# Kernel tuning notes

Measured on AMD Instinct MI355X. Metric: run time of the kernel, lower is better.

Reference implementation:

```python
import jax, jax.numpy as jnp
import numpy as np

LN_EPS = 1e-5


def layer_norm(x, gamma, beta):
    mu = jnp.mean(x, axis=-1, keepdims=True)
    var = jnp.mean(jnp.square(x - mu), axis=-1, keepdims=True)
    return (x - mu) * jax.lax.rsqrt(var + LN_EPS) * gamma + beta


def setup_inputs() -> dict:
    key = jax.random.key(0)
    ks = jax.random.split(key, 4)
    b, t, d, h, r = 4, 2048, 1024, 4096, 32
    x = jax.random.normal(ks[0], (b, t, d), dtype=jnp.float32)
    L = jax.random.normal(ks[1], (d, r), dtype=jnp.float32) * (1.0 / np.sqrt(d))
    W1 = jax.random.normal(ks[2], (d, h), dtype=jnp.float32) * (1.0 / np.sqrt(d))
    W2 = jax.random.normal(ks[3], (h, d), dtype=jnp.float32) * (1.0 / np.sqrt(h))
    return {
        "x": x, "L": L,
        "W1": W1, "b1": jnp.zeros((h,), jnp.float32),
        "W2": W2, "b2": jnp.zeros((d,), jnp.float32),
        "gamma1": jnp.ones((d,), jnp.float32), "beta1": jnp.zeros((d,), jnp.float32),
        "gamma2": jnp.ones((d,), jnp.float32), "beta2": jnp.zeros((d,), jnp.float32),
    }


def reference(x, L, W1, b1, W2, b2, gamma1, beta1, gamma2, beta2):
    d = x.shape[-1]
    # --- GeodesicAttention on norm1(x) ---
    hn = layer_norm(x, gamma1, beta1)  # (b,t,d)
    g = jnp.eye(d, dtype=x.dtype) + L @ L.T  # PSD metric G = I + L L^T, (d,d)
    # dist_sq[b,i,j] = (x_i - x_j)^T G (x_i - x_j)
    #               = q_i + q_j - 2 x_i^T G x_j   (quadratic expansion; avoids (b,t,t,d) diff tensor)
    xg = jnp.einsum('btd,de->bte', hn, g)          # G x, (b,t,d)
    q = jnp.einsum('btd,btd->bt', xg, hn)          # diag quadratic form, (b,t)
    cross = jnp.einsum('bid,bjd->bij', xg, hn)     # x_i^T G x_j, (b,t,t)
    dist_sq = q[:, :, None] + q[:, None, :] - 2.0 * cross
    attn = jax.nn.softmax(-dist_sq, axis=-1)       # (b,t,t)
    x = x + jnp.einsum('bij,bjd->bid', attn, hn)
    # --- MLP on norm2(x) ---
    hm = layer_norm(x, gamma2, beta2)
    hid = jax.nn.gelu(hm @ W1 + b1, approximate=False)
    x = x + hid @ W2 + b2
    return x
```

## Files before the change

kernel.cpp:

```cpp
#include <hip/hip_runtime.h>
#include <cstdint>

typedef float f32x4 __attribute__((ext_vector_type(4)));
typedef __bf16 bf16x8 __attribute__((ext_vector_type(8)));

#define AS1 __attribute__((address_space(1)))
#define AS3 __attribute__((address_space(3)))

__device__ __forceinline__ void gld_lds16(const void* g, void* l) {
    __builtin_amdgcn_global_load_lds((const AS1 void*)g, (AS3 void*)l, 16, 0, 0);
}

__device__ __forceinline__ unsigned short f2bf(float f) {
    unsigned u = __builtin_bit_cast(unsigned, f);
    u = u + 0x7fffu + ((u >> 16) & 1u);
    return (unsigned short)(u >> 16);
}
__device__ __forceinline__ float bf2f(unsigned short h) {
    unsigned u = ((unsigned)h) << 16;
    return __builtin_bit_cast(float, u);
}

template<int MODE>
__global__ __launch_bounds__(256) void gemm_nt(
    const unsigned short* __restrict__ A, long lda, long sAb,
    const unsigned short* __restrict__ B, long ldb, long sBb,
    void* C, long ldc, long sCb,
    const float* add, long ldadd, long sAddb,
    const float* __restrict__ bias,
    int K)
{
    __shared__ char smA[128 * 64 * 2];
    __shared__ char smB[128 * 64 * 2];
    const int tid  = threadIdx.x;
    const int lane = tid & 63, wid = tid >> 6;
    const int wr = wid >> 1, wc = wid & 1;
    const long zb = blockIdx.z;

    const int nwg  = gridDim.x * gridDim.y;
    const int orig = blockIdx.y * gridDim.x + blockIdx.x;
    const int q8 = nwg >> 3, r8 = nwg & 7;
    const int xcd = orig & 7;
    const int wg  = (xcd < r8 ? xcd * (q8 + 1) : r8 * (q8 + 1) + (xcd - r8) * q8) + (orig >> 3);
    const int bx = wg % gridDim.x, by = wg / gridDim.x;

    const char* Ab = (const char*)(A + zb * sAb + (long)by * 128 * lda);
    const char* Bb = (const char*)(B + zb * sBb + (long)bx * 128 * ldb);
    const long lda2 = lda * 2, ldb2 = ldb * 2;
    const int srow = lane >> 3;
    const int scol = (lane & 7) * 16;

    f32x4 acc[4][4] = {};
    for (int k0 = 0; k0 < K; k0 += 64) {
        if (k0) __syncthreads();
        const long kb = (long)k0 * 2;
#pragma unroll
        for (int i = 0; i < 4; ++i) {
            const int seg = i * 4 + wid;
            const int r = seg * 8 + srow;
            gld_lds16(Ab + (long)r * lda2 + kb + scol, smA + seg * 1024);
            gld_lds16(Bb + (long)r * ldb2 + kb + scol, smB + seg * 1024);
        }
        __syncthreads();
#pragma unroll
        for (int kk = 0; kk < 2; ++kk) {
            bf16x8 af[4], bfm[4];
#pragma unroll
            for (int m = 0; m < 4; ++m)
                af[m] = *(const bf16x8*)(smA + (wr * 64 + m * 16 + (lane & 15)) * 128 + kk * 64 + (lane >> 4) * 16);
#pragma unroll
            for (int n = 0; n < 4; ++n)
                bfm[n] = *(const bf16x8*)(smB + (wc * 64 + n * 16 + (lane & 15)) * 128 + kk * 64 + (lane >> 4) * 16);
#pragma unroll
            for (int m = 0; m < 4; ++m)
#pragma unroll
                for (int n = 0; n < 4; ++n)
                    acc[m][n] = __builtin_amdgcn_mfma_f32_16x16x32_bf16(af[m], bfm[n], acc[m][n], 0, 0, 0);
        }
    }
    const long row0 = (long)by * 128 + wr * 64 + (lane >> 4) * 4;
    const long col0 = (long)bx * 128 + wc * 64 + (lane & 15);
#pragma unroll
    for (int m = 0; m < 4; ++m)
#pragma unroll
        for (int n = 0; n < 4; ++n)
#pragma unroll
            for (int j = 0; j < 4; ++j) {
                const long r = row0 + m * 16 + j;
                const long c = col0 + n * 16;
                const float v = acc[m][n][j];
                if (MODE == 0) {
                    ((float*)C)[zb * sCb + r * ldc + c] = v;
                } else if (MODE == 1) {
                    ((float*)C)[zb * sCb + r * ldc + c] = v + add[zb * sAddb + r * ldadd + c];
                } else if (MODE == 2) {
                    float t = v + bias[c];
                    float gl = 0.5f * t * (1.0f + erff(t * 0.70710678118654752f));
                    ((unsigned short*)C)[zb * sCb + r * ldc + c] = f2bf(gl);
                } else {
                    ((float*)C)[zb * sCb + r * ldc + c] = v + bias[c] + add[zb * sAddb + r * ldadd + c];
                }
            }
}

__global__ __launch_bounds__(256) void ln_kernel(
    const float* __restrict__ x, const float* __restrict__ gamma, const float* __restrict__ beta,
    unsigned short* __restrict__ out, int ldout, float* qout, int pad)
{
    const int tid = threadIdx.x;
    const long row = blockIdx.x;
    float4 v = ((const float4*)(x + row * 1024))[tid];
    float s = v.x + v.y + v.z + v.w;
    float s2 = v.x * v.x + v.y * v.y + v.z * v.z + v.w * v.w;
#pragma unroll
    for (int off = 32; off; off >>= 1) {
        s  += __shfl_down(s, off);
        s2 += __shfl_down(s2, off);
    }
    __shared__ float red[12];
    const int lane = tid & 63, wid = tid >> 6;
    if (lane == 0) { red[wid] = s; red[4 + wid] = s2; }
    __syncthreads();
    s  = red[0] + red[1] + red[2] + red[3];
    s2 = red[4] + red[5] + red[6] + red[7];
    const float mu = s * (1.0f / 1024.0f);
    const float var = s2 * (1.0f / 1024.0f) - mu * mu;
    const float rs = rsqrtf(var + 1e-5f);
    const float4 g = ((const float4*)gamma)[tid];
    const float4 b = ((const float4*)beta)[tid];
    unsigned short o0 = f2bf((v.x - mu) * rs * g.x + b.x);
    unsigned short o1 = f2bf((v.y - mu) * rs * g.y + b.y);
    unsigned short o2 = f2bf((v.z - mu) * rs * g.z + b.z);
    unsigned short o3 = f2bf((v.w - mu) * rs * g.w + b.w);
    ushort4 ov; ov.x = o0; ov.y = o1; ov.z = o2; ov.w = o3;
    ((ushort4*)(out + row * (long)ldout))[tid] = ov;
    if (pad && tid < 32) out[row * (long)ldout + 1056 + tid] = 0;
    if (qout) {
        float y0 = bf2f(o0), y1 = bf2f(o1), y2 = bf2f(o2), y3 = bf2f(o3);
        float sq = y0 * y0 + y1 * y1 + y2 * y2 + y3 * y3;
#pragma unroll
        for (int off = 32; off; off >>= 1) sq += __shfl_down(sq, off);
        if (lane == 0) red[8 + wid] = sq;
        __syncthreads();
        if (tid == 0) qout[row] = red[8] + red[9] + red[10] + red[11];
    }
}

__global__ __launch_bounds__(256) void u_kernel(
    unsigned short* __restrict__ z, const float* __restrict__ L, float* __restrict__ q)
{
    const int tid = threadIdx.x;
    const long row = blockIdx.x;
    __shared__ float hn[1024];
    __shared__ float part[8][32];
    ushort4 uv = ((const ushort4*)(z + row * 1088))[tid];
    hn[tid * 4 + 0] = bf2f(uv.x);
    hn[tid * 4 + 1] = bf2f(uv.y);
    hn[tid * 4 + 2] = bf2f(uv.z);
    hn[tid * 4 + 3] = bf2f(uv.w);
    __syncthreads();
    const int j = tid & 31, grp = tid >> 5;
    float acc = 0.f;
    const float* Lp = L + j;
#pragma unroll 4
    for (int d = grp * 128; d < grp * 128 + 128; ++d)
        acc += hn[d] * Lp[(long)d * 32];
    part[grp][j] = acc;
    __syncthreads();
    if (tid < 32) {
        float u = 0.f;
#pragma unroll
        for (int g2 = 0; g2 < 8; ++g2) u += part[g2][tid];
        unsigned short ub = f2bf(u);
        z[row * 1088 + 1024 + tid] = ub;
        float uf = bf2f(ub);
        part[0][tid] = uf * uf;
    }
    __syncthreads();
    if (tid == 0) {
        float sq = 0.f;
#pragma unroll
        for (int t2 = 0; t2 < 32; ++t2) sq += part[0][t2];
        q[row] += sq;
    }
}

__global__ __launch_bounds__(256) void softmax_kernel(
    float* S, const float* qb)
{
    const int tid = threadIdx.x;
    const long i = blockIdx.x, bl = blockIdx.y;
    float* Sr = S + (bl * 2048 + i) * 2048;
    const float* qr = qb + bl * 2048;
    float l[8];
    float mx = -1e30f;
#pragma unroll
    for (int c2 = 0; c2 < 8; ++c2) {
        const int jj = tid + c2 * 256;
        l[c2] = 2.0f * Sr[jj] - qr[jj];
        mx = fmaxf(mx, l[c2]);
    }
#pragma unroll
    for (int off = 32; off; off >>= 1) mx = fmaxf(mx, __shfl_xor(mx, off));
    __shared__ float red[8];
    const int lane = tid & 63, wid = tid >> 6;
    if (lane == 0) red[wid] = mx;
    __syncthreads();
    mx = fmaxf(fmaxf(red[0], red[1]), fmaxf(red[2], red[3]));
    float sum = 0.f;
#pragma unroll
    for (int c2 = 0; c2 < 8; ++c2) { l[c2] = __expf(l[c2] - mx); sum += l[c2]; }
#pragma unroll
    for (int off = 32; off; off >>= 1) sum += __shfl_xor(sum, off);
    if (lane == 0) red[4 + wid] = sum;
    __syncthreads();
    sum = red[4] + red[5] + red[6] + red[7];
    const float inv = 1.0f / sum;
    unsigned short* Pr = (unsigned short*)S + (bl * 2048 + i) * 4096;
#pragma unroll
    for (int c2 = 0; c2 < 8; ++c2)
        Pr[tid + c2 * 256] = f2bf(l[c2] * inv);
}

__global__ __launch_bounds__(256) void transpose_v_kernel(
    const unsigned short* __restrict__ z, unsigned short* __restrict__ Vt, long sVtb)
{
    __shared__ unsigned short t[32][33];
    const int tid = threadIdx.x;
    const int tx = tid & 31, ty = tid >> 5;
    const long b = blockIdx.z;
    const long k0 = (long)blockIdx.x * 32, n0 = (long)blockIdx.y * 32;
#pragma unroll
    for (int r = 0; r < 32; r += 8)
        t[r + ty][tx] = z[(b * 2048 + k0 + r + ty) * 1088 + n0 + tx];
    __syncthreads();
#pragma unroll
    for (int r = 0; r < 32; r += 8)
        Vt[b * sVtb + (n0 + r + ty) * 2048 + k0 + tx] = t[tx][r + ty];
}

__global__ __launch_bounds__(256) void cast_transpose_kernel(
    const float* __restrict__ W, unsigned short* __restrict__ Wt, int rows, int cols)
{
    __shared__ float t[32][33];
    const int tid = threadIdx.x;
    const int tx = tid & 31, ty = tid >> 5;
    const long r0 = (long)blockIdx.y * 32, c0 = (long)blockIdx.x * 32;
#pragma unroll
    for (int r = 0; r < 32; r += 8)
        t[r + ty][tx] = W[(r0 + r + ty) * (long)cols + c0 + tx];
    __syncthreads();
#pragma unroll
    for (int r = 0; r < 32; r += 8)
        Wt[(c0 + r + ty) * (long)rows + r0 + tx] = f2bf(t[tx][r + ty]);
}

extern "C" void kernel_launch(void* const* d_in, const int* in_sizes, int n_in,
                              void* d_out, int out_size, void* d_ws, size_t ws_size,
                              hipStream_t stream)
{
    const float* x   = (const float*)d_in[0];
    const float* L   = (const float*)d_in[1];
    const float* W1  = (const float*)d_in[2];
    const float* b1  = (const float*)d_in[3];
    const float* W2  = (const float*)d_in[4];
    const float* b2  = (const float*)d_in[5];
    const float* g1  = (const float*)d_in[6];
    const float* be1 = (const float*)d_in[7];
    const float* g2  = (const float*)d_in[8];
    const float* be2 = (const float*)d_in[9];
    float* out = (float*)d_out;
    unsigned short* z = (unsigned short*)d_out;

    char* wsp = (char*)d_ws;
    float* q = (float*)wsp;
    char* pool = wsp + 32768;
    unsigned short* Vt   = (unsigned short*)pool;
    float*          Smat = (float*)(pool + 16777216);
    unsigned short* W1t = (unsigned short*)pool;
    unsigned short* W2t = (unsigned short*)(pool + 8388608);
    unsigned short* hm  = (unsigned short*)(pool + 16777216);
    unsigned short* hid = (unsigned short*)(pool + 33554432);
    const bool fullMLP = ws_size >= (size_t)32768 + 100663296 + 65536;

    ln_kernel<<<8192, 256, 0, stream>>>(x, g1, be1, z, 1088, q, 1);
    u_kernel<<<8192, 256, 0, stream>>>(z, L, q);

    transpose_v_kernel<<<dim3(64, 32, 4), 256, 0, stream>>>(z, Vt, (long)1024 * 2048);
    gemm_nt<0><<<dim3(16, 16, 4), 256, 0, stream>>>(
        z, 1088, (long)2048 * 1088,
        z, 1088, (long)2048 * 1088,
        Smat, 2048, (long)2048 * 2048,
        nullptr, 0, 0, nullptr, 1088);
    softmax_kernel<<<dim3(2048, 4), 256, 0, stream>>>(Smat, q);
    gemm_nt<1><<<dim3(8, 16, 4), 256, 0, stream>>>(
        (const unsigned short*)Smat, 4096, (long)2048 * 4096,
        Vt, 2048, (long)1024 * 2048,
        out, 1024, (long)2048 * 1024,
        x, 1024, (long)2048 * 1024,
        nullptr, 2048);

    cast_transpose_kernel<<<dim3(128, 32), 256, 0, stream>>>(W1, W1t, 1024, 4096);
    cast_transpose_kernel<<<dim3(32, 128), 256, 0, stream>>>(W2, W2t, 4096, 1024);
    ln_kernel<<<8192, 256, 0, stream>>>(out, g2, be2, hm, 1024, nullptr, 0);
    if (fullMLP) {
        gemm_nt<2><<<dim3(32, 64, 1), 256, 0, stream>>>(
            hm, 1024, 0, W1t, 1024, 0,
            hid, 4096, 0, nullptr, 0, 0, b1, 1024);
        gemm_nt<3><<<dim3(8, 64, 1), 256, 0, stream>>>(
            hid, 4096, 0, W2t, 4096, 0,
            out, 1024, 0, out, 1024, 0, b2, 4096);
    } else {
        for (int c = 0; c < 2; ++c) {
            const unsigned short* hmc = hm + (size_t)c * 4096 * 1024;
            float* oc = out + (size_t)c * 4096 * 1024;
            gemm_nt<2><<<dim3(32, 32, 1), 256, 0, stream>>>(
                hmc, 1024, 0, W1t, 1024, 0,
                hid, 4096, 0, nullptr, 0, 0, b1, 1024);
            gemm_nt<3><<<dim3(8, 32, 1), 256, 0, stream>>>(
                hid, 4096, 0, W2t, 4096, 0,
                oc, 1024, 0, oc, 1024, 0, b2, 4096);
        }
    }
}
```

Measured before the change: 425.1 us.

## Replace GEMM with 256-row tiles, 512 threads and 4-stage async LDS pipeline

Replaces the single-buffered 128x128 GEMM with a 256xBN tile kernel that runs 8 waves per block and keeps four K=32 stages in LDS. Loads are issued ahead and waited on through explicit vmcnt counts. MFMA blocks are wrapped in setprio so global loads overlap compute and the per-tile barrier stalls go away. The larger tiles raise data reuse per load. In exchange the kernel uses more LDS and registers, and correctness depends on hand-counted vmcnt values and on K being a multiple of 32.

```diff
diff --git a/kernel.cpp b/kernel.cpp
--- a/kernel.cpp
+++ b/kernel.cpp
@@ -21,22 +21,27 @@
     return __builtin_bit_cast(float, u);
 }
 
-template<int MODE>
-__global__ __launch_bounds__(256) void gemm_nt(
+__device__ __forceinline__ void bar() {
+    asm volatile("" ::: "memory");
+    __builtin_amdgcn_s_barrier();
+    asm volatile("" ::: "memory");
+}
+
+template<int BN, int MODE>
+__global__ __launch_bounds__(512, 2) void gemm_nt2(
     const unsigned short* __restrict__ A, long lda, long sAb,
     const unsigned short* __restrict__ B, long ldb, long sBb,
     void* C, long ldc, long sCb,
     const float* add, long ldadd, long sAddb,
-    const float* __restrict__ bias,
-    int K)
-{
-    __shared__ char smA[128 * 64 * 2];
-    __shared__ char smB[128 * 64 * 2];
-    const int tid  = threadIdx.x;
-    const int lane = tid & 63, wid = tid >> 6;
-    const int wr = wid >> 1, wc = wid & 1;
+    const float* __restrict__ bias, int K)
+{
+    constexpr int NR  = BN / 64;
+    constexpr int BUF = 16384 + BN * 64;
+    __shared__ char sm[4 * BUF];
+    const int tid = threadIdx.x, lane = tid & 63, wid = tid >> 6;
+    const int wr = wid >> 2, wc = wid & 3;
+
     const long zb = blockIdx.z;
-
     const int nwg  = gridDim.x * gridDim.y;
     const int orig = blockIdx.y * gridDim.x + blockIdx.x;
     const int q8 = nwg >> 3, r8 = nwg & 7;
@@ -44,46 +49,74 @@
     const int wg  = (xcd < r8 ? xcd * (q8 + 1) : r8 * (q8 + 1) + (xcd - r8) * q8) + (orig >> 3);
     const int bx = wg % gridDim.x, by = wg / gridDim.x;
 
-    const char* Ab = (const char*)(A + zb * sAb + (long)by * 128 * lda);
-    const char* Bb = (const char*)(B + zb * sBb + (long)bx * 128 * ldb);
-    const long lda2 = lda * 2, ldb2 = ldb * 2;
-    const int srow = lane >> 3;
-    const int scol = (lane & 7) * 16;
-
-    f32x4 acc[4][4] = {};
-    for (int k0 = 0; k0 < K; k0 += 64) {
-        if (k0) __syncthreads();
-        const long kb = (long)k0 * 2;
-#pragma unroll
-        for (int i = 0; i < 4; ++i) {
-            const int seg = i * 4 + wid;
-            const int r = seg * 8 + srow;
-            gld_lds16(Ab + (long)r * lda2 + kb + scol, smA + seg * 1024);
-            gld_lds16(Bb + (long)r * ldb2 + kb + scol, smB + seg * 1024);
+    const char* Ab = (const char*)(A + zb * sAb + (long)by * 256 * lda);
+    const char* Bb = (const char*)(B + zb * sBb + (long)bx * BN * ldb);
+    const long ldaB = lda * 2, ldbB = ldb * 2;
+    const int  grow = tid >> 2;
+    const long gcol = (long)(tid & 3) * 16;
+
+    auto stage = [&](int kt, int bi) {
+        const char* As = Ab + (long)kt * 64 + gcol;
+        const char* Bs = Bb + (long)kt * 64 + gcol;
+        char* d = sm + bi * BUF + wid * 1024;
+#pragma unroll
+        for (int i = 0; i < 2; ++i)
+            gld_lds16(As + (long)(i * 128 + grow) * ldaB, d + i * 8192);
+#pragma unroll
+        for (int i = 0; i < BN / 128; ++i)
+            gld_lds16(Bs + (long)(i * 128 + grow) * ldbB, d + 16384 + i * 8192);
+    };
+
+    f32x4 acc[8][NR] = {};
+    const int NT = K / 32;
+    stage(0, 0);
+    if (NT > 1) stage(1, 1);
+    if (NT > 2) stage(2, 2);
+
+    for (int t = 0; t < NT; ++t) {
+        const int rem = NT - t;
+        if (rem > 3) {
+            stage(t + 3, (t + 3) & 3);
+            if constexpr (BN == 256) asm volatile("s_waitcnt vmcnt(12)" ::: "memory");
+            else                     asm volatile("s_waitcnt vmcnt(9)"  ::: "memory");
+        } else if (rem == 3) {
+            if constexpr (BN == 256) asm volatile("s_waitcnt vmcnt(8)" ::: "memory");
+            else                     asm volatile("s_waitcnt vmcnt(6)" ::: "memory");
+        } else if (rem == 2) {
+            if constexpr (BN == 256) asm volatile("s_waitcnt vmcnt(4)" ::: "memory");
+            else                     asm volatile("s_waitcnt vmcnt(3)" ::: "memory");
+        } else {
+            asm volatile("s_waitcnt vmcnt(0)" ::: "memory");
         }
-        __syncthreads();
-#pragma unroll
-        for (int kk = 0; kk < 2; ++kk) {
-            bf16x8 af[4], bfm[4];
-#pragma unroll
-            for (int m = 0; m < 4; ++m)
-                af[m] = *(const bf16x8*)(smA + (wr * 64 + m * 16 + (lane & 15)) * 128 + kk * 64 + (lane >> 4) * 16);
-#pragma unroll
-            for (int n = 0; n < 4; ++n)
-                bfm[n] = *(const bf16x8*)(smB + (wc * 64 + n * 16 + (lane & 15)) * 128 + kk * 64 + (lane >> 4) * 16);
-#pragma unroll
-            for (int m = 0; m < 4; ++m)
-#pragma unroll
-                for (int n = 0; n < 4; ++n)
-                    acc[m][n] = __builtin_amdgcn_mfma_f32_16x16x32_bf16(af[m], bfm[n], acc[m][n], 0, 0, 0);
-        }
-    }
-    const long row0 = (long)by * 128 + wr * 64 + (lane >> 4) * 4;
-    const long col0 = (long)bx * 128 + wc * 64 + (lane & 15);
-#pragma unroll
-    for (int m = 0; m < 4; ++m)
-#pragma unroll
-        for (int n = 0; n < 4; ++n)
+        bar();
+
+        const char* bufA = sm + (t & 3) * BUF;
+        const char* bufB = bufA + 16384;
+        bf16x8 af[8], bfr[NR];
+#pragma unroll
+        for (int m = 0; m < 8; ++m)
+            af[m] = *(const bf16x8*)(bufA + (wr * 128 + m * 16 + (lane & 15)) * 64 + (lane >> 4) * 16);
+#pragma unroll
+        for (int n = 0; n < NR; ++n)
+            bfr[n] = *(const bf16x8*)(bufB + (wc * 16 * NR + n * 16 + (lane & 15)) * 64 + (lane >> 4) * 16);
+        __builtin_amdgcn_s_setprio(1);
+#pragma unroll
+        for (int m = 0; m < 8; ++m)
+#pragma unroll
+            for (int n = 0; n < NR; ++n)
+                acc[m][n] = __builtin_amdgcn_mfma_f32_16x16x32_bf16(af[m], bfr[n], acc[m][n], 0, 0, 0);
+        __builtin_amdgcn_s_setprio(0);
+        asm volatile("s_waitcnt lgkmcnt(0)" ::: "memory");
+        __builtin_amdgcn_sched_barrier(0);
+        bar();
+    }
+
+    const long row0 = (long)by * 256 + wr * 128 + (lane >> 4) * 4;
+    const long col0 = (long)bx * BN + wc * 16 * NR + (lane & 15);
+#pragma unroll
+    for (int m = 0; m < 8; ++m)
+#pragma unroll
+        for (int n = 0; n < NR; ++n)
 #pragma unroll
             for (int j = 0; j < 4; ++j) {
                 const long r = row0 + m * 16 + j;
@@ -94,8 +127,8 @@
                 } else if (MODE == 1) {
                     ((float*)C)[zb * sCb + r * ldc + c] = v + add[zb * sAddb + r * ldadd + c];
                 } else if (MODE == 2) {
-                    float t = v + bias[c];
-                    float gl = 0.5f * t * (1.0f + erff(t * 0.70710678118654752f));
+                    float tt = v + bias[c];
+                    float gl = 0.5f * tt * (1.0f + erff(tt * 0.70710678118654752f));
                     ((unsigned short*)C)[zb * sCb + r * ldc + c] = f2bf(gl);
                 } else {
                     ((float*)C)[zb * sCb + r * ldc + c] = v + bias[c] + add[zb * sAddb + r * ldadd + c];
@@ -287,13 +320,13 @@
     u_kernel<<<8192, 256, 0, stream>>>(z, L, q);
 
     transpose_v_kernel<<<dim3(64, 32, 4), 256, 0, stream>>>(z, Vt, (long)1024 * 2048);
-    gemm_nt<0><<<dim3(16, 16, 4), 256, 0, stream>>>(
+    gemm_nt2<256, 0><<<dim3(8, 8, 4), 512, 0, stream>>>(
         z, 1088, (long)2048 * 1088,
         z, 1088, (long)2048 * 1088,
         Smat, 2048, (long)2048 * 2048,
         nullptr, 0, 0, nullptr, 1088);
     softmax_kernel<<<dim3(2048, 4), 256, 0, stream>>>(Smat, q);
-    gemm_nt<1><<<dim3(8, 16, 4), 256, 0, stream>>>(
+    gemm_nt2<128, 1><<<dim3(8, 8, 4), 512, 0, stream>>>(
         (const unsigned short*)Smat, 4096, (long)2048 * 4096,
         Vt, 2048, (long)1024 * 2048,
         out, 1024, (long)2048 * 1024,
@@ -304,20 +337,20 @@
     cast_transpose_kernel<<<dim3(32, 128), 256, 0, stream>>>(W2, W2t, 4096, 1024);
     ln_kernel<<<8192, 256, 0, stream>>>(out, g2, be2, hm, 1024, nullptr, 0);
     if (fullMLP) {
-        gemm_nt<2><<<dim3(32, 64, 1), 256, 0, stream>>>(
+        gemm_nt2<256, 2><<<dim3(16, 32, 1), 512, 0, stream>>>(
             hm, 1024, 0, W1t, 1024, 0,
             hid, 4096, 0, nullptr, 0, 0, b1, 1024);
-        gemm_nt<3><<<dim3(8, 64, 1), 256, 0, stream>>>(
+        gemm_nt2<128, 3><<<dim3(8, 32, 1), 512, 0, stream>>>(
             hid, 4096, 0, W2t, 4096, 0,
             out, 1024, 0, out, 1024, 0, b2, 4096);
     } else {
         for (int c = 0; c < 2; ++c) {
             const unsigned short* hmc = hm + (size_t)c * 4096 * 1024;
             float* oc = out + (size_t)c * 4096 * 1024;
-            gemm_nt<2><<<dim3(32, 32, 1), 256, 0, stream>>>(
+            gemm_nt2<256, 2><<<dim3(16, 16, 1), 512, 0, stream>>>(
                 hmc, 1024, 0, W1t, 1024, 0,
                 hid, 4096, 0, nullptr, 0, 0, b1, 1024);
-            gemm_nt<3><<<dim3(8, 32, 1), 256, 0, stream>>>(
+            gemm_nt2<128, 3><<<dim3(8, 16, 1), 512, 0, stream>>>(
                 hid, 4096, 0, W2t, 4096, 0,
                 oc, 1024, 0, oc, 1024, 0, b2, 4096);
         }
```

New measurement: 392.8 us. 1.08x faster.

## Triple-buffer GEMM K-loop with async LDS loads and swizzled shared layout

Applied to the files above, without the earlier changes.

Rewrites the bf16 MFMA GEMM main loop to use a 3-stage LDS ring buffer with a K step of 32. Global-to-LDS loads for tile t+2 are issued before the MFMAs on tile t, and explicit vmcnt waits replace the double syncthreads per iteration. It also adds an XOR swizzle on the LDS layout to cut bank conflicts, raises wave priority around the MFMA block, and sets an occupancy hint of 3 blocks per CU. The aim is to hide global memory latency behind compute. In exchange it uses more shared memory and depends on hand-tuned waitcnt counts being correct.

```diff
diff --git a/kernel.cpp b/kernel.cpp
--- a/kernel.cpp
+++ b/kernel.cpp
@@ -21,22 +21,31 @@
     return __builtin_bit_cast(float, u);
 }
 
+__device__ __forceinline__ void bar() {
+    asm volatile("" ::: "memory");
+    __builtin_amdgcn_s_barrier();
+    asm volatile("" ::: "memory");
+}
+
+#define WAITVM(n) asm volatile("s_waitcnt vmcnt(" #n ")" ::: "memory")
+#define LGKM0     asm volatile("s_waitcnt lgkmcnt(0)" ::: "memory")
+#define SCHED0    __builtin_amdgcn_sched_barrier(0)
+
 template<int MODE>
-__global__ __launch_bounds__(256) void gemm_nt(
+__global__ __launch_bounds__(256, 3) void gemm128(
     const unsigned short* __restrict__ A, long lda, long sAb,
     const unsigned short* __restrict__ B, long ldb, long sBb,
     void* C, long ldc, long sCb,
     const float* add, long ldadd, long sAddb,
-    const float* __restrict__ bias,
-    int K)
-{
-    __shared__ char smA[128 * 64 * 2];
-    __shared__ char smB[128 * 64 * 2];
-    const int tid  = threadIdx.x;
-    const int lane = tid & 63, wid = tid >> 6;
+    const float* __restrict__ bias, int K)
+{
+    constexpr int ABUF = 128 * 64;
+    constexpr int BUF  = 2 * ABUF;
+    __shared__ char sm[3 * BUF];
+    const int tid = threadIdx.x, lane = tid & 63, wid = tid >> 6;
     const int wr = wid >> 1, wc = wid & 1;
+
     const long zb = blockIdx.z;
-
     const int nwg  = gridDim.x * gridDim.y;
     const int orig = blockIdx.y * gridDim.x + blockIdx.x;
     const int q8 = nwg >> 3, r8 = nwg & 7;
@@ -46,38 +55,58 @@
 
     const char* Ab = (const char*)(A + zb * sAb + (long)by * 128 * lda);
     const char* Bb = (const char*)(B + zb * sBb + (long)bx * 128 * ldb);
-    const long lda2 = lda * 2, ldb2 = ldb * 2;
-    const int srow = lane >> 3;
-    const int scol = (lane & 7) * 16;
+    const long ldaB = lda * 2, ldbB = ldb * 2;
+
+    const long gsw = (long)(((tid & 3) ^ ((tid >> 3) & 3)) << 4);
+    auto stage = [&](int kt, int b) {
+#pragma unroll
+        for (int i = 0; i < 2; ++i) {
+            const int r = i * 64 + (tid >> 2);
+            gld_lds16(Ab + (long)r * ldaB + (long)kt * 64 + gsw,
+                      sm + b * BUF + i * 4096 + wid * 1024);
+            gld_lds16(Bb + (long)r * ldbB + (long)kt * 64 + gsw,
+                      sm + b * BUF + ABUF + i * 4096 + wid * 1024);
+        }
+    };
 
     f32x4 acc[4][4] = {};
-    for (int k0 = 0; k0 < K; k0 += 64) {
-        if (k0) __syncthreads();
-        const long kb = (long)k0 * 2;
-#pragma unroll
-        for (int i = 0; i < 4; ++i) {
-            const int seg = i * 4 + wid;
-            const int r = seg * 8 + srow;
-            gld_lds16(Ab + (long)r * lda2 + kb + scol, smA + seg * 1024);
-            gld_lds16(Bb + (long)r * ldb2 + kb + scol, smB + seg * 1024);
-        }
-        __syncthreads();
-#pragma unroll
-        for (int kk = 0; kk < 2; ++kk) {
-            bf16x8 af[4], bfm[4];
-#pragma unroll
-            for (int m = 0; m < 4; ++m)
-                af[m] = *(const bf16x8*)(smA + (wr * 64 + m * 16 + (lane & 15)) * 128 + kk * 64 + (lane >> 4) * 16);
+    const int NT = K / 32;
+    const int cc = ((lane >> 4) ^ ((lane >> 1) & 3)) << 4;
+
+    stage(0, 0); stage(1, 1);
+    WAITVM(4);
+    bar();
+
+#pragma unroll 1
+    for (int t = 0; t < NT; ++t) {
+        const char* bufp = sm + (t % 3) * BUF;
+        bf16x8 af[4], bfr[4];
+#pragma unroll
+        for (int m = 0; m < 4; ++m) {
+            const int R = wr * 64 + m * 16 + (lane & 15);
+            af[m] = *(const bf16x8*)(bufp + R * 64 + cc);
+        }
+#pragma unroll
+        for (int n = 0; n < 4; ++n) {
+            const int R = wc * 64 + n * 16 + (lane & 15);
+            bfr[n] = *(const bf16x8*)(bufp + ABUF + R * 64 + cc);
+        }
+        if (t + 2 < NT) stage(t + 2, (t + 2) % 3);
+        LGKM0; SCHED0;
+        __builtin_amdgcn_s_setprio(1);
+#pragma unroll
+        for (int m = 0; m < 4; ++m)
 #pragma unroll
             for (int n = 0; n < 4; ++n)
-                bfm[n] = *(const bf16x8*)(smB + (wc * 64 + n * 16 + (lane & 15)) * 128 + kk * 64 + (lane >> 4) * 16);
-#pragma unroll
-            for (int m = 0; m < 4; ++m)
-#pragma unroll
-                for (int n = 0; n < 4; ++n)
-                    acc[m][n] = __builtin_amdgcn_mfma_f32_16x16x32_bf16(af[m], bfm[n], acc[m][n], 0, 0, 0);
-        }
-    }
+                acc[m][n] = __builtin_amdgcn_mfma_f32_16x16x32_bf16(
+                    af[m], bfr[n], acc[m][n], 0, 0, 0);
+        __builtin_amdgcn_s_setprio(0);
+        if (t + 1 < NT) {
+            if (t + 2 < NT) WAITVM(4); else WAITVM(0);
+            bar();
+        }
+    }
+
     const long row0 = (long)by * 128 + wr * 64 + (lane >> 4) * 4;
     const long col0 = (long)bx * 128 + wc * 64 + (lane & 15);
 #pragma unroll
@@ -94,8 +123,8 @@
                 } else if (MODE == 1) {
                     ((float*)C)[zb * sCb + r * ldc + c] = v + add[zb * sAddb + r * ldadd + c];
                 } else if (MODE == 2) {
-                    float t = v + bias[c];
-                    float gl = 0.5f * t * (1.0f + erff(t * 0.70710678118654752f));
+                    float tt = v + bias[c];
+                    float gl = 0.5f * tt * (1.0f + erff(tt * 0.70710678118654752f));
                     ((unsigned short*)C)[zb * sCb + r * ldc + c] = f2bf(gl);
                 } else {
                     ((float*)C)[zb * sCb + r * ldc + c] = v + bias[c] + add[zb * sAddb + r * ldadd + c];
@@ -287,13 +316,13 @@
     u_kernel<<<8192, 256, 0, stream>>>(z, L, q);
 
     transpose_v_kernel<<<dim3(64, 32, 4), 256, 0, stream>>>(z, Vt, (long)1024 * 2048);
-    gemm_nt<0><<<dim3(16, 16, 4), 256, 0, stream>>>(
+    gemm128<0><<<dim3(16, 16, 4), 256, 0, stream>>>(
         z, 1088, (long)2048 * 1088,
         z, 1088, (long)2048 * 1088,
         Smat, 2048, (long)2048 * 2048,
         nullptr, 0, 0, nullptr, 1088);
     softmax_kernel<<<dim3(2048, 4), 256, 0, stream>>>(Smat, q);
-    gemm_nt<1><<<dim3(8, 16, 4), 256, 0, stream>>>(
+    gemm128<1><<<dim3(8, 16, 4), 256, 0, stream>>>(
         (const unsigned short*)Smat, 4096, (long)2048 * 4096,
         Vt, 2048, (long)1024 * 2048,
         out, 1024, (long)2048 * 1024,
@@ -304,20 +333,20 @@
     cast_transpose_kernel<<<dim3(32, 128), 256, 0, stream>>>(W2, W2t, 4096, 1024);
     ln_kernel<<<8192, 256, 0, stream>>>(out, g2, be2, hm, 1024, nullptr, 0);
     if (fullMLP) {
-        gemm_nt<2><<<dim3(32, 64, 1), 256, 0, stream>>>(
+        gemm128<2><<<dim3(32, 64, 1), 256, 0, stream>>>(
             hm, 1024, 0, W1t, 1024, 0,
             hid, 4096, 0, nullptr, 0, 0, b1, 1024);
-        gemm_nt<3><<<dim3(8, 64, 1), 256, 0, stream>>>(
+        gemm128<3><<<dim3(8, 64, 1), 256, 0, stream>>>(
             hid, 4096, 0, W2t, 4096, 0,
             out, 1024, 0, out, 1024, 0, b2, 4096);
     } else {
         for (int c = 0; c < 2; ++c) {
             const unsigned short* hmc = hm + (size_t)c * 4096 * 1024;
             float* oc = out + (size_t)c * 4096 * 1024;
-            gemm_nt<2><<<dim3(32, 32, 1), 256, 0, stream>>>(
+            gemm128<2><<<dim3(32, 32, 1), 256, 0, stream>>>(
                 hmc, 1024, 0, W1t, 1024, 0,
                 hid, 4096, 0, nullptr, 0, 0, b1, 1024);
-            gemm_nt<3><<<dim3(8, 32, 1), 256, 0, stream>>>(
+            gemm128<3><<<dim3(8, 32, 1), 256, 0, stream>>>(
                 hid, 4096, 0, W2t, 4096, 0,
                 oc, 1024, 0, oc, 1024, 0, b2, 4096);
         }
```

Measured after the change: 392.6 us. 1.08x faster.
